# Kernel tuning notes

Measured on AMD Instinct MI355X. Metric: run time of the kernel, lower is better.

## Reference

```python
import jax, jax.numpy as jnp
import numpy as np

B, T, I, H, O = 4096, 512, 1, 64, 3

def setup_inputs() -> dict:
    key = jax.random.key(0)
    ks = jax.random.split(key, 7)
    s = 1.0 / np.sqrt(H)  # torch default LSTM init scale
    return {
        "x": jax.random.normal(ks[0], (B, T, I), dtype=jnp.float32),
        "W_ih": jax.random.uniform(ks[1], (4 * H, I), jnp.float32, -s, s),
        "W_hh": jax.random.uniform(ks[2], (4 * H, H), jnp.float32, -s, s),
        "b_ih": jax.random.uniform(ks[3], (4 * H,), jnp.float32, -s, s),
        "b_hh": jax.random.uniform(ks[4], (4 * H,), jnp.float32, -s, s),
        "W_out": jax.random.uniform(ks[5], (O, H), jnp.float32, -s, s),
        "b_out": jax.random.uniform(ks[6], (O,), jnp.float32, -s, s),
    }

def reference(x, W_ih, W_hh, b_ih, b_hh, W_out, b_out):
    # Single-layer LSTM (PyTorch gate order i,f,g,o), zero initial state,
    # then linear head applied to the last hidden state (== r_out[:, -1, :]).
    b = b_ih + b_hh
    Bsz, Hh = x.shape[0], W_hh.shape[1]
    # Precompute input projections for all timesteps: [T, B, 4H]
    x_proj = jnp.einsum('bti,gi->tbg', x, W_ih) + b

    def step(carry, xp_t):
        h, c = carry
        gates = xp_t + h @ W_hh.T  # [B, 4H]
        i, f, g, o = jnp.split(gates, 4, axis=-1)
        c_new = jax.nn.sigmoid(f) * c + jax.nn.sigmoid(i) * jnp.tanh(g)
        h_new = jax.nn.sigmoid(o) * jnp.tanh(c_new)
        return (h_new, c_new), None

    h0 = jnp.zeros((Bsz, Hh), x.dtype)
    (h_last, _), _ = jax.lax.scan(step, (h0, h0), x_proj)
    return h_last @ W_out.T + b_out  # [B, 3]
```

## Files before the change

### kernel.cpp

```cpp
#include <hip/hip_runtime.h>

#define BATCH 4096
#define TT 512
#define HH 64
#define BT 4
#define XS 516
#define HS 72

typedef __attribute__((ext_vector_type(8))) short short8;
typedef __attribute__((ext_vector_type(4))) float floatx4;

__device__ __forceinline__ unsigned short f2bf(float f) {
    unsigned u = __float_as_uint(f);
    u = u + 0x7FFFu + ((u >> 16) & 1u);
    return (unsigned short)(u >> 16);
}

__global__ __launch_bounds__(256, 4) void lstm_kernel(
    const float* __restrict__ x, const float* __restrict__ W_ih,
    const float* __restrict__ W_hh, const float* __restrict__ b_ih,
    const float* __restrict__ b_hh, const float* __restrict__ W_out,
    const float* __restrict__ b_out, float* __restrict__ out)
{
    __shared__ __align__(16) float x_s[BT * XS];
    __shared__ __align__(16) unsigned short hb0[16 * HS];
    __shared__ __align__(16) unsigned short hb1[16 * HS];
    __shared__ __align__(16) float hf[BT * 65];

    const int tid = threadIdx.x;
    const int w = tid >> 6;
    const int l = tid & 63;
    const int q = l >> 4;
    const int c = l & 15;
    const int n = 16 * w + c;
    const int bbase = blockIdx.x * BT;

    for (int i = 0; i < 2; ++i) {
        int flat = i * 256 + tid;
        int row = flat >> 7, c4 = flat & 127;
        const float4* xg = reinterpret_cast<const float4*>(x + (size_t)(bbase + row) * TT);
        float4 v = xg[c4];
        *reinterpret_cast<float4*>(&x_s[row * XS + c4 * 4]) = v;
    }
    for (int i = tid; i < 16 * HS; i += 256) { hb0[i] = 0; hb1[i] = 0; }

    short8 bfr[4][2];
    float wih[4], bb[4];
    for (int t = 0; t < 4; ++t) {
        int g = 64 * t + n;
        wih[t] = W_ih[g];
        bb[t] = b_ih[g] + b_hh[g];
        for (int ks = 0; ks < 2; ++ks) {
            const float* wp = W_hh + g * 64 + ks * 32 + q * 8;
            short8 v;
            #pragma unroll
            for (int j = 0; j < 8; ++j) v[j] = (short)f2bf(wp[j]);
            bfr[t][ks] = v;
        }
    }

    float cst = 0.f;
    float hv = 0.f;
    floatx4 acc[4];
    #pragma unroll
    for (int t = 0; t < 4; ++t) acc[t] = floatx4{0.f, 0.f, 0.f, 0.f};

    const int aoff = c * HS + q * 8;
    const int woff = (4 * q) * HS + n;
    const float* xrow = &x_s[q * XS];
    const float L1 = 1.44269504089f;
    const float L2 = 2.88539008178f;

    __syncthreads();

    auto step = [&](const unsigned short* __restrict__ src,
                    unsigned short* __restrict__ dst, float xv) {
        short8 a0 = *reinterpret_cast<const short8*>(src + aoff);
        short8 a1 = *reinterpret_cast<const short8*>(src + aoff + 32);
        #pragma unroll
        for (int t = 0; t < 4; ++t) acc[t][0] = fmaf(xv, wih[t], bb[t]);
        #pragma unroll
        for (int t = 0; t < 4; ++t) {
            acc[t] = __builtin_amdgcn_mfma_f32_16x16x32_bf16(a0, bfr[t][0], acc[t], 0, 0, 0);
            acc[t] = __builtin_amdgcn_mfma_f32_16x16x32_bf16(a1, bfr[t][1], acc[t], 0, 0, 0);
        }
        float gi = acc[0][0], gf = acc[1][0], gg = acc[2][0], go = acc[3][0];
        float ei = __builtin_amdgcn_exp2f(-L1 * gi);
        float ef = __builtin_amdgcn_exp2f(-L1 * gf);
        float eg = __builtin_amdgcn_exp2f( L2 * gg);
        float eo = __builtin_amdgcn_exp2f(-L1 * go);
        float pf1 = 1.f + ef, pi1 = 1.f + ei, pg1 = 1.f + eg, po1 = 1.f + eo;
        float pig = pi1 * pg1;
        float num = fmaf(cst, pig, (eg - 1.f) * pf1);
        cst = num * __builtin_amdgcn_rcpf(pf1 * pig);
        float ec = __builtin_amdgcn_exp2f(L2 * cst);
        hv = (ec - 1.f) * __builtin_amdgcn_rcpf(po1 * (1.f + ec));
        dst[woff] = f2bf(hv);
        __syncthreads();
    };

    for (int ts4 = 0; ts4 < TT; ts4 += 4) {
        float4 xq = *reinterpret_cast<const float4*>(xrow + ts4);
        step(hb0, hb1, xq.x);
        step(hb1, hb0, xq.y);
        step(hb0, hb1, xq.z);
        step(hb1, hb0, xq.w);
    }

    hf[q * 65 + n] = hv;
    __syncthreads();

    if (tid < BT * 3) {
        int row = tid / 3, o = tid % 3;
        float s = b_out[o];
        #pragma unroll 8
        for (int k = 0; k < HH; ++k) s = fmaf(hf[row * 65 + k], W_out[o * 64 + k], s);
        out[(size_t)(bbase + row) * 3 + o] = s;
    }
}

extern "C" void kernel_launch(void* const* d_in, const int* in_sizes, int n_in,
                              void* d_out, int out_size, void* d_ws, size_t ws_size,
                              hipStream_t stream) {
    const float* x     = (const float*)d_in[0];
    const float* W_ih  = (const float*)d_in[1];
    const float* W_hh  = (const float*)d_in[2];
    const float* b_ih  = (const float*)d_in[3];
    const float* b_hh  = (const float*)d_in[4];
    const float* W_out = (const float*)d_in[5];
    const float* b_out = (const float*)d_in[6];
    float* out = (float*)d_out;
    hipLaunchKernelGGL(lstm_kernel, dim3(BATCH / BT), dim3(256), 0, stream,
                       x, W_ih, W_hh, b_ih, b_hh, W_out, b_out, out);
}
```

Measured before the change: 306.3 us.

## Give each wave eight batch rows with all gates and interleave two groups

Each wave now owns 8 batch rows as two groups of 4 and computes all 256 gate columns itself. The recurrent hidden state stays in a wave-private LDS buffer, so the per-timestep block-wide barriers go away. The MFMA phase of one group is interleaved with the activation phase of the other to hide MFMA and transcendental latency. In exchange, register use rises to roughly 256+ VGPRs and only 256 blocks of 128 threads launch, which leaves about half the SIMDs idle and puts more serial MFMA work on each wave.

Measured after the change: 791.0 us. 158% more time.

```diff
diff --git a/kernel.cpp b/kernel.cpp
--- a/kernel.cpp
+++ b/kernel.cpp
@@ -3,7 +3,6 @@
 #define BATCH 4096
 #define TT 512
 #define HH 64
-#define BT 4
 #define XS 516
 #define HS 72
 
@@ -16,40 +15,41 @@
     return (unsigned short)(u >> 16);
 }
 
-__global__ __launch_bounds__(256, 4) void lstm_kernel(
+__global__ __launch_bounds__(128, 1) void lstm_kernel(
     const float* __restrict__ x, const float* __restrict__ W_ih,
     const float* __restrict__ W_hh, const float* __restrict__ b_ih,
     const float* __restrict__ b_hh, const float* __restrict__ W_out,
     const float* __restrict__ b_out, float* __restrict__ out)
 {
-    __shared__ __align__(16) float x_s[BT * XS];
-    __shared__ __align__(16) unsigned short hb0[16 * HS];
-    __shared__ __align__(16) unsigned short hb1[16 * HS];
-    __shared__ __align__(16) float hf[BT * 65];
+    __shared__ __align__(16) float x_s[16 * XS];
+    __shared__ __align__(16) unsigned short hls[2][2][16 * HS];
+    __shared__ __align__(16) float hf[16 * 65];
 
     const int tid = threadIdx.x;
     const int w = tid >> 6;
     const int l = tid & 63;
     const int q = l >> 4;
     const int c = l & 15;
-    const int n = 16 * w + c;
-    const int bbase = blockIdx.x * BT;
+    const int bbase = blockIdx.x * 16;
 
-    for (int i = 0; i < 2; ++i) {
-        int flat = i * 256 + tid;
+    for (int i = 0; i < 16; ++i) {
+        int flat = i * 128 + tid;
         int row = flat >> 7, c4 = flat & 127;
         const float4* xg = reinterpret_cast<const float4*>(x + (size_t)(bbase + row) * TT);
         float4 v = xg[c4];
         *reinterpret_cast<float4*>(&x_s[row * XS + c4 * 4]) = v;
     }
-    for (int i = tid; i < 16 * HS; i += 256) { hb0[i] = 0; hb1[i] = 0; }
+    for (int i = tid; i < 2 * 2 * 16 * HS; i += 128)
+        (&hls[0][0][0])[i] = 0;
 
-    short8 bfr[4][2];
-    float wih[4], bb[4];
-    for (int t = 0; t < 4; ++t) {
-        int g = 64 * t + n;
+    float wih[16], bb[16];
+    short8 bfr[16][2];
+    #pragma unroll
+    for (int t = 0; t < 16; ++t) {
+        int g = 16 * t + c;
         wih[t] = W_ih[g];
         bb[t] = b_ih[g] + b_hh[g];
+        #pragma unroll
         for (int ks = 0; ks < 2; ++ks) {
             const float* wp = W_hh + g * 64 + ks * 32 + q * 8;
             short8 v;
@@ -59,58 +59,71 @@
         }
     }
 
-    float cst = 0.f;
-    float hv = 0.f;
-    floatx4 acc[4];
+    floatx4 accA[16], accB[16];
     #pragma unroll
-    for (int t = 0; t < 4; ++t) acc[t] = floatx4{0.f, 0.f, 0.f, 0.f};
+    for (int t = 0; t < 16; ++t) { accA[t] = floatx4{0.f,0.f,0.f,0.f}; accB[t] = floatx4{0.f,0.f,0.f,0.f}; }
+    float cstA[4] = {0,0,0,0}, cstB[4] = {0,0,0,0};
+    float hvA[4], hvB[4];
 
+    unsigned short* hA = hls[w][0];
+    unsigned short* hB = hls[w][1];
     const int aoff = c * HS + q * 8;
-    const int woff = (4 * q) * HS + n;
-    const float* xrow = &x_s[q * XS];
+    const int woff = 4 * q * HS + c;
+    const float* xrowA = &x_s[(8 * w + q) * XS];
+    const float* xrowB = &x_s[(8 * w + 4 + q) * XS];
     const float L1 = 1.44269504089f;
     const float L2 = 2.88539008178f;
 
     __syncthreads();
 
-    auto step = [&](const unsigned short* __restrict__ src,
-                    unsigned short* __restrict__ dst, float xv) {
-        short8 a0 = *reinterpret_cast<const short8*>(src + aoff);
-        short8 a1 = *reinterpret_cast<const short8*>(src + aoff + 32);
+    auto mfma_step = [&](floatx4* acc, const unsigned short* hbuf, float xv) {
+        short8 a0 = *reinterpret_cast<const short8*>(hbuf + aoff);
+        short8 a1 = *reinterpret_cast<const short8*>(hbuf + aoff + 32);
         #pragma unroll
-        for (int t = 0; t < 4; ++t) acc[t][0] = fmaf(xv, wih[t], bb[t]);
+        for (int t = 0; t < 16; ++t) acc[t][0] = fmaf(xv, wih[t], bb[t]);
         #pragma unroll
-        for (int t = 0; t < 4; ++t) {
+        for (int t = 0; t < 16; ++t) {
             acc[t] = __builtin_amdgcn_mfma_f32_16x16x32_bf16(a0, bfr[t][0], acc[t], 0, 0, 0);
             acc[t] = __builtin_amdgcn_mfma_f32_16x16x32_bf16(a1, bfr[t][1], acc[t], 0, 0, 0);
         }
-        float gi = acc[0][0], gf = acc[1][0], gg = acc[2][0], go = acc[3][0];
-        float ei = __builtin_amdgcn_exp2f(-L1 * gi);
-        float ef = __builtin_amdgcn_exp2f(-L1 * gf);
-        float eg = __builtin_amdgcn_exp2f( L2 * gg);
-        float eo = __builtin_amdgcn_exp2f(-L1 * go);
-        float pf1 = 1.f + ef, pi1 = 1.f + ei, pg1 = 1.f + eg, po1 = 1.f + eo;
-        float pig = pi1 * pg1;
-        float num = fmaf(cst, pig, (eg - 1.f) * pf1);
-        cst = num * __builtin_amdgcn_rcpf(pf1 * pig);
-        float ec = __builtin_amdgcn_exp2f(L2 * cst);
-        hv = (ec - 1.f) * __builtin_amdgcn_rcpf(po1 * (1.f + ec));
-        dst[woff] = f2bf(hv);
-        __syncthreads();
+    };
+    auto act_step = [&](floatx4* acc, float* cst, float* hv, unsigned short* hbuf) {
+        #pragma unroll
+        for (int s = 0; s < 4; ++s) {
+            float gi = acc[s][0], gf = acc[4 + s][0], gg = acc[8 + s][0], go = acc[12 + s][0];
+            float ei = __builtin_amdgcn_exp2f(-L1 * gi);
+            float ef = __builtin_amdgcn_exp2f(-L1 * gf);
+            float eg = __builtin_amdgcn_exp2f( L2 * gg);
+            float eo = __builtin_amdgcn_exp2f(-L1 * go);
+            float pf1 = 1.f + ef, pig = (1.f + ei) * (1.f + eg);
+            float num = fmaf(cst[s], pig, (eg - 1.f) * pf1);
+            cst[s] = num * __builtin_amdgcn_rcpf(pf1 * pig);
+            float ec = __builtin_amdgcn_exp2f(L2 * cst[s]);
+            float h = (ec - 1.f) * __builtin_amdgcn_rcpf((1.f + eo) * (1.f + ec));
+            hv[s] = h;
+            hbuf[woff + 16 * s] = f2bf(h);
+        }
     };
 
-    for (int ts4 = 0; ts4 < TT; ts4 += 4) {
-        float4 xq = *reinterpret_cast<const float4*>(xrow + ts4);
-        step(hb0, hb1, xq.x);
-        step(hb1, hb0, xq.y);
-        step(hb0, hb1, xq.z);
-        step(hb1, hb0, xq.w);
+    mfma_step(accA, hA, xrowA[0]);
+    for (int k = 0; k < TT - 1; ++k) {
+        mfma_step(accB, hB, xrowB[k]);
+        act_step(accA, cstA, hvA, hA);
+        mfma_step(accA, hA, xrowA[k + 1]);
+        act_step(accB, cstB, hvB, hB);
     }
+    mfma_step(accB, hB, xrowB[TT - 1]);
+    act_step(accA, cstA, hvA, hA);
+    act_step(accB, cstB, hvB, hB);
 
-    hf[q * 65 + n] = hv;
+    #pragma unroll
+    for (int s = 0; s < 4; ++s) {
+        hf[(8 * w + q) * 65 + 16 * s + c] = hvA[s];
+        hf[(8 * w + 4 + q) * 65 + 16 * s + c] = hvB[s];
+    }
     __syncthreads();
 
-    if (tid < BT * 3) {
+    if (tid < 16 * 3) {
         int row = tid / 3, o = tid % 3;
         float s = b_out[o];
         #pragma unroll 8
@@ -130,6 +143,6 @@
     const float* W_out = (const float*)d_in[5];
     const float* b_out = (const float*)d_in[6];
     float* out = (float*)d_out;
-    hipLaunchKernelGGL(lstm_kernel, dim3(BATCH / BT), dim3(256), 0, stream,
+    hipLaunchKernelGGL(lstm_kernel, dim3(BATCH / 16), dim3(128), 0, stream,
                        x, W_ih, W_hh, b_ih, b_hh, W_out, b_out, out);
 }
```

## Pack two batch rows per MFMA lane to double batch tile per block

Applied to the files above, without the earlier changes.

Doubles the batch tile from 4 to 8 rows per block. Each lane now handles two of its MFMA output rows, with two cell states and two hidden states, so the 16-row MFMA tile carries more real work per instruction. This halves the grid, and with it the total MFMA and barrier work across the GPU. The costs are double the transcendental math per lane per step, more registers, and fewer resident blocks per CU (launch bounds lowered to 2), which gives less latency hiding on the serial recurrence.

Result: faster. 294.1 us (-4.0%).

```diff
diff --git a/kernel.cpp b/kernel.cpp
--- a/kernel.cpp
+++ b/kernel.cpp
@@ -3,7 +3,7 @@
 #define BATCH 4096
 #define TT 512
 #define HH 64
-#define BT 4
+#define BT 8
 #define XS 516
 #define HS 72
 
@@ -16,7 +16,7 @@
     return (unsigned short)(u >> 16);
 }
 
-__global__ __launch_bounds__(256, 4) void lstm_kernel(
+__global__ __launch_bounds__(256, 2) void lstm_kernel(
     const float* __restrict__ x, const float* __restrict__ W_ih,
     const float* __restrict__ W_hh, const float* __restrict__ b_ih,
     const float* __restrict__ b_hh, const float* __restrict__ W_out,
@@ -35,7 +35,7 @@
     const int n = 16 * w + c;
     const int bbase = blockIdx.x * BT;
 
-    for (int i = 0; i < 2; ++i) {
+    for (int i = 0; i < 4; ++i) {
         int flat = i * 256 + tid;
         int row = flat >> 7, c4 = flat & 127;
         const float4* xg = reinterpret_cast<const float4*>(x + (size_t)(bbase + row) * TT);
@@ -59,55 +59,67 @@
         }
     }
 
-    float cst = 0.f;
-    float hv = 0.f;
+    float cst[2] = {0.f, 0.f};
+    float hvk[2] = {0.f, 0.f};
+
     floatx4 acc[4];
     #pragma unroll
     for (int t = 0; t < 4; ++t) acc[t] = floatx4{0.f, 0.f, 0.f, 0.f};
 
     const int aoff = c * HS + q * 8;
     const int woff = (4 * q) * HS + n;
-    const float* xrow = &x_s[q * XS];
+    const float* xrowA = &x_s[(2 * q) * XS];
+    const float* xrowB = &x_s[(2 * q + 1) * XS];
     const float L1 = 1.44269504089f;
     const float L2 = 2.88539008178f;
 
     __syncthreads();
 
-    auto step = [&](const unsigned short* __restrict__ src,
-                    unsigned short* __restrict__ dst, float xv) {
-        short8 a0 = *reinterpret_cast<const short8*>(src + aoff);
-        short8 a1 = *reinterpret_cast<const short8*>(src + aoff + 32);
+    for (int ts4 = 0; ts4 < TT; ts4 += 4) {
+        float4 xa = *reinterpret_cast<const float4*>(xrowA + ts4);
+        float4 xb = *reinterpret_cast<const float4*>(xrowB + ts4);
         #pragma unroll
-        for (int t = 0; t < 4; ++t) acc[t][0] = fmaf(xv, wih[t], bb[t]);
-        #pragma unroll
-        for (int t = 0; t < 4; ++t) {
-            acc[t] = __builtin_amdgcn_mfma_f32_16x16x32_bf16(a0, bfr[t][0], acc[t], 0, 0, 0);
-            acc[t] = __builtin_amdgcn_mfma_f32_16x16x32_bf16(a1, bfr[t][1], acc[t], 0, 0, 0);
+        for (int u = 0; u < 4; ++u) {
+            const unsigned short* src = (u & 1) ? hb1 : hb0;
+            unsigned short* dst = (u & 1) ? hb0 : hb1;
+
+            short8 a0 = *reinterpret_cast<const short8*>(src + aoff);
+            short8 a1 = *reinterpret_cast<const short8*>(src + aoff + 32);
+
+            float x0 = (&xa.x)[u], x1 = (&xb.x)[u];
+            #pragma unroll
+            for (int t = 0; t < 4; ++t) {
+                acc[t][0] = fmaf(x0, wih[t], bb[t]);
+                acc[t][1] = fmaf(x1, wih[t], bb[t]);
+            }
+
+            #pragma unroll
+            for (int t = 0; t < 4; ++t) {
+                acc[t] = __builtin_amdgcn_mfma_f32_16x16x32_bf16(a0, bfr[t][0], acc[t], 0, 0, 0);
+                acc[t] = __builtin_amdgcn_mfma_f32_16x16x32_bf16(a1, bfr[t][1], acc[t], 0, 0, 0);
+            }
+
+            #pragma unroll
+            for (int rr = 0; rr < 2; ++rr) {
+                float gi = acc[0][rr], gf = acc[1][rr], gg = acc[2][rr], go = acc[3][rr];
+                float ei = __builtin_amdgcn_exp2f(-L1 * gi);
+                float ef = __builtin_amdgcn_exp2f(-L1 * gf);
+                float eg = __builtin_amdgcn_exp2f( L2 * gg);
+                float eo = __builtin_amdgcn_exp2f(-L1 * go);
+                float pf1 = 1.f + ef, pig = (1.f + ei) * (1.f + eg);
+                float num = fmaf(cst[rr], pig, (eg - 1.f) * pf1);
+                cst[rr] = num * __builtin_amdgcn_rcpf(pf1 * pig);
+                float ec = __builtin_amdgcn_exp2f(L2 * cst[rr]);
+                float hv = (ec - 1.f) * __builtin_amdgcn_rcpf((1.f + eo) * (1.f + ec));
+                hvk[rr] = hv;
+                dst[woff + rr * HS] = f2bf(hv);
+            }
+            __syncthreads();
         }
-        float gi = acc[0][0], gf = acc[1][0], gg = acc[2][0], go = acc[3][0];
-        float ei = __builtin_amdgcn_exp2f(-L1 * gi);
-        float ef = __builtin_amdgcn_exp2f(-L1 * gf);
-        float eg = __builtin_amdgcn_exp2f( L2 * gg);
-        float eo = __builtin_amdgcn_exp2f(-L1 * go);
-        float pf1 = 1.f + ef, pi1 = 1.f + ei, pg1 = 1.f + eg, po1 = 1.f + eo;
-        float pig = pi1 * pg1;
-        float num = fmaf(cst, pig, (eg - 1.f) * pf1);
-        cst = num * __builtin_amdgcn_rcpf(pf1 * pig);
-        float ec = __builtin_amdgcn_exp2f(L2 * cst);
-        hv = (ec - 1.f) * __builtin_amdgcn_rcpf(po1 * (1.f + ec));
-        dst[woff] = f2bf(hv);
-        __syncthreads();
-    };
-
-    for (int ts4 = 0; ts4 < TT; ts4 += 4) {
-        float4 xq = *reinterpret_cast<const float4*>(xrow + ts4);
-        step(hb0, hb1, xq.x);
-        step(hb1, hb0, xq.y);
-        step(hb0, hb1, xq.z);
-        step(hb1, hb0, xq.w);
     }
 
-    hf[q * 65 + n] = hv;
+    hf[(2 * q) * 65 + n] = hvk[0];
+    hf[(2 * q + 1) * 65 + n] = hvk[1];
     __syncthreads();
 
     if (tid < BT * 3) {
```
